# Performance work log

Hardware: AMD Instinct MI355X
Metric: run time of the kernel (lower is better)

## Reference

```python
import jax, jax.numpy as jnp
import numpy as np

TEMPERATURE = 0.1


def setup_inputs() -> dict:
    key = jax.random.key(0)
    k1, k2 = jax.random.split(key)
    N, D = 8192, 128
    features = jax.random.normal(k1, (N, D), dtype=jnp.float32)
    labels = jax.random.randint(k2, (N,), 0, 1000, dtype=jnp.int64)
    return {"features": features, "labels": labels}


def reference(features, labels):
    N = features.shape[0]
    # L2-normalize rows
    feats = features / jnp.linalg.norm(features, axis=1, keepdims=True)
    # positive-pair mask from labels [N, N]
    labels = labels.reshape(-1, 1)
    mask = (labels == labels.T).astype(feats.dtype)
    # similarity matrix scaled by temperature
    sim = jnp.matmul(feats, feats.T) / TEMPERATURE
    # exclude self-comparisons (diagonal)
    logits_mask = 1.0 - jnp.eye(N, dtype=feats.dtype)
    mask = mask * logits_mask
    exp_logits = jnp.exp(sim) * logits_mask
    log_prob = sim - jnp.log(exp_logits.sum(axis=1, keepdims=True) + 1e-9)
    mask_sum = mask.sum(axis=1)
    mask_sum = jnp.where(mask_sum == 0, jnp.ones_like(mask_sum), mask_sum)
    mean_log_prob_pos = (mask * log_prob).sum(axis=1) / mask_sum
    return -mean_log_prob_pos.mean()
```

## Files before the change

kernel.cpp:

```cpp
#include <hip/hip_runtime.h>
#include <hip/hip_bf16.h>
#include <math.h>


constexpr int N = 8192;
constexpr int D = 128;

typedef __attribute__((ext_vector_type(8))) short short8;
typedef __attribute__((ext_vector_type(4))) float f32x4;

__device__ __forceinline__ float fast_exp2(float x) {
#if __has_builtin(__builtin_amdgcn_exp2f)
    return __builtin_amdgcn_exp2f(x);
#else
    return __expf(x * 0.69314718056f);
#endif
}

__device__ __forceinline__ void gload_lds16(const void* g, void* s) {
    __builtin_amdgcn_global_load_lds(
        (const __attribute__((address_space(1))) unsigned int*)g,
        (__attribute__((address_space(3))) unsigned int*)s, 16, 0, 0);
}

__device__ __forceinline__ void stage_tile(const unsigned short* __restrict__ src,
                                           unsigned short* dst, int row0,
                                           int w, int lr, int lq) {
#pragma unroll
    for (int it = 0; it < 8; ++it) {
        int rbase = w * 32 + it * 4;
        int r = rbase + lr;
        int q = lq ^ (r & 7);
        gload_lds16(src + ((size_t)(row0 + r) * D + q * 8), dst + rbase * D);
    }
}

__global__ void zero_kernel(int* __restrict__ hist) {
    hist[threadIdx.x] = 0;
}

__global__ void prep_kernel(const float* __restrict__ F,
                            const int* __restrict__ labels,
                            unsigned short* __restrict__ Fb,
                            float* __restrict__ rowExp,
                            float* __restrict__ rowPos,
                            int* __restrict__ hist) {
    int row = blockIdx.x * 4 + (threadIdx.x >> 6);
    int l = threadIdx.x & 63;
    float2 v = ((const float2*)(F + (size_t)row * D))[l];
    float ss = v.x * v.x + v.y * v.y;
#pragma unroll
    for (int off = 32; off > 0; off >>= 1) ss += __shfl_xor(ss, off);
    float sc = sqrtf(14.4269504089f / ss);
    __hip_bfloat16 hx = __float2bfloat16(v.x * sc);
    __hip_bfloat16 hy = __float2bfloat16(v.y * sc);
    ushort2 u;
    u.x = *(unsigned short*)&hx;
    u.y = *(unsigned short*)&hy;
    ((ushort2*)(Fb + (size_t)row * D))[l] = u;
    if (l == 0) {
        rowExp[row] = 0.0f;
        rowPos[row] = 0.0f;
        atomicAdd(&hist[labels[row]], 1);
    }
}

__global__ __launch_bounds__(256, 2) void sim_kernel(
    const unsigned short* __restrict__ Fb, const int* __restrict__ labels,
    float* __restrict__ rowExp, float* __restrict__ rowPos) {
    __shared__ unsigned short At[128 * D];
    __shared__ unsigned short Bt[128 * D];

    int bid = blockIdx.x, q = 0, base = 0;
    while (bid >= base + 4 * (16 - q)) { base += 4 * (16 - q); ++q; }
    int rem = bid - base, ng = 16 - q;
    int ti = 4 * q + rem / ng;
    int g = 15 - (rem % ng);
    int tjs = max(ti, 4 * g), tje = 4 * g + 3;
    const int i0 = ti * 128;

    const int t = threadIdx.x, w = t >> 6, l = t & 63;
    const int lr = l >> 4, lq = l & 15;
    const int c = l & 15, quad = l >> 4;
    const int wy = w >> 1, wx = w & 1;

    stage_tile(Fb, At, i0, w, lr, lq);
    stage_tile(Fb, Bt, tjs * 128, w, lr, lq);

    int li[4][4];
#pragma unroll
    for (int m = 0; m < 4; ++m)
#pragma unroll
        for (int r = 0; r < 4; ++r)
            li[m][r] = labels[i0 + wy * 64 + m * 16 + quad * 4 + r];

    float RE[4][4] = {}, RP[4][4] = {};

    for (int tj = tjs; tj <= tje; ++tj) {
        __syncthreads();
        int j0 = tj * 128;
        f32x4 acc[4][4] = {};
#pragma unroll
        for (int kk = 0; kk < 4; ++kk) {
            short8 af[4], bf[4];
            int sl = (kk * 4 + quad) ^ (c & 7);
#pragma unroll
            for (int m = 0; m < 4; ++m) {
                af[m] = *(const short8*)&At[(wy * 64 + m * 16 + c) * D + sl * 8];
                bf[m] = *(const short8*)&Bt[(wx * 64 + m * 16 + c) * D + sl * 8];
            }
#pragma unroll
            for (int m = 0; m < 4; ++m)
#pragma unroll
                for (int n = 0; n < 4; ++n)
                    acc[m][n] = __builtin_amdgcn_mfma_f32_16x16x32_bf16(
                        af[m], bf[n], acc[m][n], 0, 0, 0);
        }
        __syncthreads();
        if (tj < tje) stage_tile(Fb, Bt, (tj + 1) * 128, w, lr, lq);

        int lj[4];
#pragma unroll
        for (int n = 0; n < 4; ++n) lj[n] = labels[j0 + wx * 64 + n * 16 + c];
        const bool diag = (tj == ti);
        float ce[4] = {}, cp[4] = {};
#pragma unroll
        for (int m = 0; m < 4; ++m) {
#pragma unroll
            for (int n = 0; n < 4; ++n) {
#pragma unroll
                for (int r = 0; r < 4; ++r) {
                    float s2 = acc[m][n][r];
                    bool self = diag && ((wy * 64 + m * 16 + quad * 4 + r) ==
                                         (wx * 64 + n * 16 + c));
                    float e = self ? 0.0f : fast_exp2(s2);
                    float p = (!self && li[m][r] == lj[n]) ? s2 : 0.0f;
                    RE[m][r] += e;
                    RP[m][r] += p;
                    ce[n] += e;
                    cp[n] += p;
                }
            }
        }
        if (!diag) {
#pragma unroll
            for (int n = 0; n < 4; ++n) {
                ce[n] += __shfl_xor(ce[n], 16);
                ce[n] += __shfl_xor(ce[n], 32);
                cp[n] += __shfl_xor(cp[n], 16);
                cp[n] += __shfl_xor(cp[n], 32);
            }
            if (quad == 0) {
#pragma unroll
                for (int n = 0; n < 4; ++n) {
                    int gj = j0 + wx * 64 + n * 16 + c;
                    atomicAdd(&rowExp[gj], ce[n]);
                    atomicAdd(&rowPos[gj], cp[n]);
                }
            }
        }
    }

#pragma unroll
    for (int m = 0; m < 4; ++m)
#pragma unroll
        for (int r = 0; r < 4; ++r) {
#pragma unroll
            for (int off = 1; off < 16; off <<= 1) {
                RE[m][r] += __shfl_xor(RE[m][r], off);
                RP[m][r] += __shfl_xor(RP[m][r], off);
            }
        }
    if (c == 0) {
#pragma unroll
        for (int m = 0; m < 4; ++m)
#pragma unroll
            for (int r = 0; r < 4; ++r) {
                int gi = i0 + wy * 64 + m * 16 + quad * 4 + r;
                atomicAdd(&rowExp[gi], RE[m][r]);
                atomicAdd(&rowPos[gi], RP[m][r]);
            }
    }
}

__global__ void finalize_kernel(const float* __restrict__ rowExp,
                                const float* __restrict__ rowPos,
                                const int* __restrict__ labels,
                                const int* __restrict__ hist,
                                float* __restrict__ out) {
    int t = threadIdx.x;
    float a = 0.0f;
    for (int i = t; i < N; i += 1024) {
        int cnt = hist[labels[i]] - 1;
        if (cnt > 0)
            a += logf(rowExp[i] + 1e-9f) -
                 0.69314718056f * rowPos[i] / (float)cnt;
    }
#pragma unroll
    for (int off = 32; off > 0; off >>= 1) a += __shfl_xor(a, off);
    __shared__ float ws16[16];
    if ((t & 63) == 0) ws16[t >> 6] = a;
    __syncthreads();
    if (t == 0) {
        float s = 0.0f;
#pragma unroll
        for (int i = 0; i < 16; ++i) s += ws16[i];
        out[0] = s / (float)N;
    }
}

extern "C" void kernel_launch(void* const* d_in, const int* in_sizes, int n_in,
                              void* d_out, int out_size, void* d_ws, size_t ws_size,
                              hipStream_t stream) {
    const float* F      = (const float*)d_in[0];
    const int*   labels = (const int*)d_in[1];
    float* out = (float*)d_out;

    unsigned short* Fb = (unsigned short*)d_ws;
    float* rowExp = (float*)(Fb + (size_t)N * D);
    float* rowPos = rowExp + N;
    int*   hist   = (int*)(rowPos + N);

    zero_kernel<<<1, 1024, 0, stream>>>(hist);
    prep_kernel<<<N / 4, 256, 0, stream>>>(F, labels, Fb, rowExp, rowPos, hist);
    sim_kernel<<<544, 256, 0, stream>>>(Fb, labels, rowExp, rowPos);
    finalize_kernel<<<1, 1024, 0, stream>>>(rowExp, rowPos, labels, hist, out);
}
```

Baseline: 102.9 us.

## Double-buffer B tiles, keep A fragments in registers, move histogram to finalize LDS

The A-tile fragments are now loaded once into registers, which frees the second LDS buffer so the B tiles can be double-buffered. The next B tile is prefetched before the MFMA loop, overlapping the global-to-LDS copy with compute. The epilogue is split into diagonal and off-diagonal paths so the self-mask check disappears from the common case. The label histogram is built in shared memory inside finalize, which removes the zero kernel and the global atomics in prep. The cost is 64 extra VGPRs for the A fragments, which may press on occupancy under the two-blocks-per-CU launch bound.

```diff
diff --git a/kernel.cpp b/kernel.cpp
--- a/kernel.cpp
+++ b/kernel.cpp
@@ -35,16 +35,10 @@
     }
 }
 
-__global__ void zero_kernel(int* __restrict__ hist) {
-    hist[threadIdx.x] = 0;
-}
-
 __global__ void prep_kernel(const float* __restrict__ F,
-                            const int* __restrict__ labels,
                             unsigned short* __restrict__ Fb,
                             float* __restrict__ rowExp,
-                            float* __restrict__ rowPos,
-                            int* __restrict__ hist) {
+                            float* __restrict__ rowPos) {
     int row = blockIdx.x * 4 + (threadIdx.x >> 6);
     int l = threadIdx.x & 63;
     float2 v = ((const float2*)(F + (size_t)row * D))[l];
@@ -61,15 +55,14 @@
     if (l == 0) {
         rowExp[row] = 0.0f;
         rowPos[row] = 0.0f;
-        atomicAdd(&hist[labels[row]], 1);
     }
 }
 
 __global__ __launch_bounds__(256, 2) void sim_kernel(
     const unsigned short* __restrict__ Fb, const int* __restrict__ labels,
     float* __restrict__ rowExp, float* __restrict__ rowPos) {
-    __shared__ unsigned short At[128 * D];
-    __shared__ unsigned short Bt[128 * D];
+    __shared__ unsigned short B0[128 * D];
+    __shared__ unsigned short B1[128 * D];
 
     int bid = blockIdx.x, q = 0, base = 0;
     while (bid >= base + 4 * (16 - q)) { base += 4 * (16 - q); ++q; }
@@ -84,8 +77,8 @@
     const int c = l & 15, quad = l >> 4;
     const int wy = w >> 1, wx = w & 1;
 
-    stage_tile(Fb, At, i0, w, lr, lq);
-    stage_tile(Fb, Bt, tjs * 128, w, lr, lq);
+    stage_tile(Fb, B0, i0, w, lr, lq);
+    stage_tile(Fb, B1, tjs * 128, w, lr, lq);
 
     int li[4][4];
 #pragma unroll
@@ -94,55 +87,83 @@
         for (int r = 0; r < 4; ++r)
             li[m][r] = labels[i0 + wy * 64 + m * 16 + quad * 4 + r];
 
+    __syncthreads();
+
+    short8 Af[4][4];
+#pragma unroll
+    for (int kk = 0; kk < 4; ++kk) {
+        int sl = (kk * 4 + quad) ^ (c & 7);
+#pragma unroll
+        for (int m = 0; m < 4; ++m)
+            Af[kk][m] = *(const short8*)&B0[(wy * 64 + m * 16 + c) * D + sl * 8];
+    }
+
+    __syncthreads();
+
     float RE[4][4] = {}, RP[4][4] = {};
 
     for (int tj = tjs; tj <= tje; ++tj) {
-        __syncthreads();
-        int j0 = tj * 128;
+        const int it = tj - tjs;
+        unsigned short* curB = (it & 1) ? B0 : B1;
+        unsigned short* nxtB = (it & 1) ? B1 : B0;
+        if (tj < tje) stage_tile(Fb, nxtB, (tj + 1) * 128, w, lr, lq);
+
+        const int j0 = tj * 128;
+        int lj[4];
+#pragma unroll
+        for (int n = 0; n < 4; ++n) lj[n] = labels[j0 + wx * 64 + n * 16 + c];
+
         f32x4 acc[4][4] = {};
 #pragma unroll
         for (int kk = 0; kk < 4; ++kk) {
-            short8 af[4], bf[4];
+            short8 bf[4];
             int sl = (kk * 4 + quad) ^ (c & 7);
 #pragma unroll
-            for (int m = 0; m < 4; ++m) {
-                af[m] = *(const short8*)&At[(wy * 64 + m * 16 + c) * D + sl * 8];
-                bf[m] = *(const short8*)&Bt[(wx * 64 + m * 16 + c) * D + sl * 8];
-            }
+            for (int m = 0; m < 4; ++m)
+                bf[m] = *(const short8*)&curB[(wx * 64 + m * 16 + c) * D + sl * 8];
 #pragma unroll
             for (int m = 0; m < 4; ++m)
 #pragma unroll
                 for (int n = 0; n < 4; ++n)
                     acc[m][n] = __builtin_amdgcn_mfma_f32_16x16x32_bf16(
-                        af[m], bf[n], acc[m][n], 0, 0, 0);
+                        Af[kk][m], bf[n], acc[m][n], 0, 0, 0);
         }
-        __syncthreads();
-        if (tj < tje) stage_tile(Fb, Bt, (tj + 1) * 128, w, lr, lq);
-
-        int lj[4];
-#pragma unroll
-        for (int n = 0; n < 4; ++n) lj[n] = labels[j0 + wx * 64 + n * 16 + c];
-        const bool diag = (tj == ti);
-        float ce[4] = {}, cp[4] = {};
-#pragma unroll
-        for (int m = 0; m < 4; ++m) {
-#pragma unroll
-            for (int n = 0; n < 4; ++n) {
-#pragma unroll
-                for (int r = 0; r < 4; ++r) {
-                    float s2 = acc[m][n][r];
-                    bool self = diag && ((wy * 64 + m * 16 + quad * 4 + r) ==
-                                         (wx * 64 + n * 16 + c));
-                    float e = self ? 0.0f : fast_exp2(s2);
-                    float p = (!self && li[m][r] == lj[n]) ? s2 : 0.0f;
-                    RE[m][r] += e;
-                    RP[m][r] += p;
-                    ce[n] += e;
-                    cp[n] += p;
+
+        if (tj == ti) {
+#pragma unroll
+            for (int m = 0; m < 4; ++m) {
+#pragma unroll
+                for (int n = 0; n < 4; ++n) {
+#pragma unroll
+                    for (int r = 0; r < 4; ++r) {
+                        float s2 = acc[m][n][r];
+                        bool self = (wy * 64 + m * 16 + quad * 4 + r) ==
+                                    (wx * 64 + n * 16 + c);
+                        float e = self ? 0.0f : fast_exp2(s2);
+                        float p = (!self && li[m][r] == lj[n]) ? s2 : 0.0f;
+                        RE[m][r] += e;
+                        RP[m][r] += p;
+                    }
                 }
             }
-        }
-        if (!diag) {
+        } else {
+            float ce[4] = {}, cp[4] = {};
+#pragma unroll
+            for (int m = 0; m < 4; ++m) {
+#pragma unroll
+                for (int n = 0; n < 4; ++n) {
+#pragma unroll
+                    for (int r = 0; r < 4; ++r) {
+                        float s2 = acc[m][n][r];
+                        float e = fast_exp2(s2);
+                        float p = (li[m][r] == lj[n]) ? s2 : 0.0f;
+                        RE[m][r] += e;
+                        RP[m][r] += p;
+                        ce[n] += e;
+                        cp[n] += p;
+                    }
+                }
+            }
 #pragma unroll
             for (int n = 0; n < 4; ++n) {
                 ce[n] += __shfl_xor(ce[n], 16);
@@ -159,6 +180,8 @@
                 }
             }
         }
+
+        if (tj < tje) __syncthreads();
     }
 
 #pragma unroll
@@ -186,19 +209,30 @@
 __global__ void finalize_kernel(const float* __restrict__ rowExp,
                                 const float* __restrict__ rowPos,
                                 const int* __restrict__ labels,
-                                const int* __restrict__ hist,
                                 float* __restrict__ out) {
+    __shared__ int hist[1024];
+    __shared__ float ws16[16];
     int t = threadIdx.x;
+    hist[t] = 0;
+    __syncthreads();
+    int lab[8];
+#pragma unroll
+    for (int k = 0; k < 8; ++k) {
+        lab[k] = labels[t + 1024 * k];
+        atomicAdd(&hist[lab[k]], 1);
+    }
+    __syncthreads();
     float a = 0.0f;
-    for (int i = t; i < N; i += 1024) {
-        int cnt = hist[labels[i]] - 1;
+#pragma unroll
+    for (int k = 0; k < 8; ++k) {
+        int i = t + 1024 * k;
+        int cnt = hist[lab[k]] - 1;
         if (cnt > 0)
             a += logf(rowExp[i] + 1e-9f) -
                  0.69314718056f * rowPos[i] / (float)cnt;
     }
 #pragma unroll
     for (int off = 32; off > 0; off >>= 1) a += __shfl_xor(a, off);
-    __shared__ float ws16[16];
     if ((t & 63) == 0) ws16[t >> 6] = a;
     __syncthreads();
     if (t == 0) {
@@ -219,10 +253,8 @@
     unsigned short* Fb = (unsigned short*)d_ws;
     float* rowExp = (float*)(Fb + (size_t)N * D);
     float* rowPos = rowExp + N;
-    int*   hist   = (int*)(rowPos + N);
-
-    zero_kernel<<<1, 1024, 0, stream>>>(hist);
-    prep_kernel<<<N / 4, 256, 0, stream>>>(F, labels, Fb, rowExp, rowPos, hist);
+
+    prep_kernel<<<N / 4, 256, 0, stream>>>(F, Fb, rowExp, rowPos);
     sim_kernel<<<544, 256, 0, stream>>>(Fb, labels, rowExp, rowPos);
-    finalize_kernel<<<1, 1024, 0, stream>>>(rowExp, rowPos, labels, hist, out);
-}
+    finalize_kernel<<<1, 1024, 0, stream>>>(rowExp, rowPos, labels, out);
+}
```

Measured after the change: 160.0 us. 1.56x slower.
